# Performance work log

Hardware: AMD Instinct MI355X
Metric: run time of the kernel (lower is better)

The kernel has to match this reference:

```python
import jax, jax.numpy as jnp
import numpy as np

N_HEADS = 8
D_HEAD = 64  # n_embd=512 / n_heads=8


def setup_inputs() -> dict:
    key = jax.random.key(0)
    ks = jax.random.split(key, 5)
    B, T, C = 2, 4096, 512
    x = jax.random.normal(ks[0], (B, T, C), dtype=jnp.float32)
    s = 1.0 / np.sqrt(C)
    Wq = jax.random.normal(ks[1], (C, C), dtype=jnp.float32) * s
    Wk = jax.random.normal(ks[2], (C, C), dtype=jnp.float32) * s
    Wv = jax.random.normal(ks[3], (C, C), dtype=jnp.float32) * s
    Wout = jax.random.normal(ks[4], (C, C), dtype=jnp.float32) * s
    return {"x": x, "Wq": Wq, "Wk": Wk, "Wv": Wv, "Wout": Wout}


def reference(x, Wq, Wk, Wv, Wout):
    # x: [B,T,C]; nn.Linear(y) = y @ W.T, here weights stored as [C,C] used directly
    B, T, C = x.shape
    H, D = N_HEADS, D_HEAD
    q = (x @ Wq.T).reshape(B, T, H, D).transpose(0, 2, 1, 3)  # [B,H,T,D]
    k = (x @ Wk.T).reshape(B, T, H, D).transpose(0, 2, 1, 3)
    v = (x @ Wv.T).reshape(B, T, H, D).transpose(0, 2, 1, 3)
    att = jnp.einsum('bhqd,bhkd->bhqk', q, k) / jnp.sqrt(jnp.float32(D))  # [B,H,T,T]
    causal = jnp.tril(jnp.ones((T, T), dtype=bool))
    att = jnp.where(causal, att, -jnp.inf)
    att = jax.nn.softmax(att, axis=-1)
    # dropout is identity in eval mode (p=0)
    y = jnp.einsum('bhqk,bhkd->bhqd', att, v)  # [B,H,T,D]
    y = y.transpose(0, 2, 1, 3).reshape(B, T, C)
    return y @ Wout.T
```

## Files before the change

kernel.cpp:

```cpp
#include <hip/hip_runtime.h>
#include <hip/hip_bf16.h>
#include <math.h>
#include <stdint.h>

using bf16 = __hip_bfloat16;
typedef __attribute__((ext_vector_type(8))) short short8;
typedef __attribute__((ext_vector_type(4))) short short4v;
typedef __attribute__((ext_vector_type(4))) float float4v;

#define MFMA16(a, b, c) __builtin_amdgcn_mfma_f32_16x16x32_bf16(a, b, c, 0, 0, 0)

__device__ __forceinline__ short bfbits(float f) {
  bf16 h = (bf16)f;
  return *(short*)&h;
}

__device__ __forceinline__ short8 ld_cvt8(const float* p) {
  union { float4v v[2]; float f[8]; } u;
  u.v[0] = *(const float4v*)p;
  u.v[1] = *(const float4v*)(p + 4);
  short8 r;
#pragma unroll
  for (int j = 0; j < 8; j++) r[j] = bfbits(u.f[j]);
  return r;
}

__device__ __forceinline__ void gload16(const bf16* g, bf16* l) {
  __builtin_amdgcn_global_load_lds(
      (const __attribute__((address_space(1))) void*)g,
      (__attribute__((address_space(3))) void*)l, 16, 0, 0);
}

__global__ __launch_bounds__(256) void conv_all(
    const float* __restrict__ x, const float* __restrict__ w0,
    const float* __restrict__ w1, const float* __restrict__ w2,
    const float* __restrict__ w3, bf16* __restrict__ cx,
    bf16* __restrict__ cw) {
  size_t gid = ((size_t)blockIdx.x * 256 + threadIdx.x) * 8;
  const float* src;
  bf16* dst;
  size_t off;
  if (gid < 4194304) {
    src = x; dst = cx; off = gid;
  } else {
    size_t r = gid - 4194304;
    int wi = (int)(r >> 18);
    src = wi == 0 ? w0 : wi == 1 ? w1 : wi == 2 ? w2 : w3;
    dst = cw + ((size_t)wi << 18);
    off = r & 262143;
  }
  *(short8*)(dst + off) = ld_cvt8(src + off);
}

template <int MODE, int MT>
__device__ __forceinline__ void gemm_body(bf16* As, bf16* Bs,
                                          const bf16* __restrict__ A,
                                          const bf16* __restrict__ W,
                                          void* __restrict__ outp,
                                          float oscale) {
  constexpr int MI = MT / 32;
  const int bm = blockIdx.x * MT, bn = blockIdx.y * 128;
  const int tid = threadIdx.x;
  const int lane = tid & 63;
  const int wave = tid >> 6;
  const int lr = lane & 15, quad = lane >> 4;
  const int wm = (wave & 1) * (MT / 2), wn = (wave >> 1) * 64;

  const int srow = lane >> 3;
  const int scl = (lane & 7) ^ (srow & 7);
  const int rsw = lr & 7;

  float4v acc[MI][4] = {};

  for (int k0 = 0; k0 < 512; k0 += 64) {
    __syncthreads();
#pragma unroll
    for (int j = 0; j < MT / 32; j++) {
      const int m = wave + 4 * j;
      gload16(&A[(size_t)(bm + 8 * m + srow) * 512 + k0 + scl * 8],
              &As[(8 * m) * 64]);
    }
#pragma unroll
    for (int j = 0; j < 4; j++) {
      const int m = wave + 4 * j;
      gload16(&W[(size_t)(bn + 8 * m + srow) * 512 + k0 + scl * 8],
              &Bs[(8 * m) * 64]);
    }
    __syncthreads();
#pragma unroll
    for (int kk = 0; kk < 2; kk++) {
      short8 af[MI], bfv[4];
#pragma unroll
      for (int i = 0; i < MI; i++)
        af[i] = *(const short8*)
            &As[(wm + i * 16 + lr) * 64 + ((4 * kk + quad) ^ rsw) * 8];
#pragma unroll
      for (int i = 0; i < 4; i++)
        bfv[i] = *(const short8*)
            &Bs[(wn + i * 16 + lr) * 64 + ((4 * kk + quad) ^ rsw) * 8];
#pragma unroll
      for (int mi = 0; mi < MI; mi++)
#pragma unroll
        for (int ni = 0; ni < 4; ni++)
          acc[mi][ni] = MFMA16(af[mi], bfv[ni], acc[mi][ni]);
    }
  }

  const int row0 = bm + wm + quad * 4;
  const int col0 = bn + wn + lr;
#pragma unroll
  for (int mi = 0; mi < MI; mi++) {
#pragma unroll
    for (int ni = 0; ni < 4; ni++) {
      const int col = col0 + ni * 16;
      if (MODE == 1) {
        float* out = (float*)outp;
#pragma unroll
        for (int i = 0; i < 4; i++) {
          int m = row0 + mi * 16 + i;
          out[(size_t)m * 512 + col] = acc[mi][ni][i];
        }
      } else if (MODE == 0) {
        bf16* out = (bf16*)outp;
        const int hh = col >> 6, d = col & 63;
#pragma unroll
        for (int i = 0; i < 4; i++) {
          int m = row0 + mi * 16 + i;
          int bb = m >> 12, t = m & 4095;
          out[(((size_t)(bb * 8 + hh) * 4096 + t) << 6) + d] =
              (bf16)(acc[mi][ni][i] * oscale);
        }
      } else {
        bf16* out = (bf16*)outp;
        const int hh = col >> 6, d = col & 63;
        int m0 = row0 + mi * 16;
        int bb = m0 >> 12, t0 = m0 & 4095;
        short4v pk;
#pragma unroll
        for (int i = 0; i < 4; i++) pk[i] = bfbits(acc[mi][ni][i]);
        *(short4v*)&out[(((size_t)(bb * 8 + hh) * 64 + d) << 12) + t0] = pk;
      }
    }
  }
}

#define QSCALE 0.18033688f

__global__ __launch_bounds__(256) void qkv_kernel(
    const bf16* __restrict__ cx, const bf16* __restrict__ cW,
    bf16* q, bf16* k, bf16* vt) {
  __shared__ __align__(16) bf16 As[128 * 64];
  __shared__ __align__(16) bf16 Bs[128 * 64];
  if (blockIdx.z == 0)      gemm_body<0, 128>(As, Bs, cx, cW, q, QSCALE);
  else if (blockIdx.z == 1) gemm_body<0, 128>(As, Bs, cx, cW + 262144, k, 1.0f);
  else                      gemm_body<2, 128>(As, Bs, cx, cW + 2 * 262144, vt, 1.0f);
}

__global__ __launch_bounds__(256) void proj_kernel(
    const bf16* __restrict__ y, const bf16* __restrict__ cWout,
    float* __restrict__ out) {
  __shared__ __align__(16) bf16 As[64 * 64];
  __shared__ __align__(16) bf16 Bs[128 * 64];
  gemm_body<1, 64>(As, Bs, y, cWout, out, 1.0f);
}

__device__ __forceinline__ int lsw(int row, int col) {
  return (row << 6) + (col ^ ((row & 7) << 3));
}

template <bool DIAG>
__device__ __forceinline__ void attn_step(const bf16* __restrict__ Kc,
                                          const bf16* __restrict__ Vc,
                                          short8 qf0, short8 qf1, short8 ones,
                                          int wave, int lr, int quad,
                                          float4v& Lacc, float4v* O) {
  float4v S[4] = {};
#pragma unroll
  for (int nc = 0; nc < 4; nc++) {
    short8 kf0 = *(const short8*)&Kc[lsw(nc * 16 + lr, quad * 8)];
    short8 kf1 = *(const short8*)&Kc[lsw(nc * 16 + lr, 32 + quad * 8)];
    S[nc] = MFMA16(kf0, qf0, S[nc]);
    S[nc] = MFMA16(kf1, qf1, S[nc]);
  }

  short8 pf0, pf1;
#pragma unroll
  for (int nc = 0; nc < 4; nc++) {
#pragma unroll
    for (int i = 0; i < 4; i++) {
      float pv = exp2f(S[nc][i]);
      if (DIAG) {
        int kl = nc * 16 + quad * 4 + i;
        pv = (kl > wave * 16 + lr) ? 0.f : pv;
      }
      short bb = bfbits(pv);
      if (nc == 0)      pf0[i] = bb;
      else if (nc == 1) pf0[4 + i] = bb;
      else if (nc == 2) pf1[i] = bb;
      else              pf1[4 + i] = bb;
    }
  }

  Lacc = MFMA16(pf0, ones, Lacc);
  Lacc = MFMA16(pf1, ones, Lacc);

#pragma unroll
  for (int nc = 0; nc < 4; nc++) {
    const int row = nc * 16 + lr;
    short8 vfa = *(const short8*)&Vc[lsw(row, quad * 8)];
    short8 vfb = *(const short8*)&Vc[lsw(row, 32 + quad * 8)];
    O[nc] = MFMA16(pf0, vfa, O[nc]);
    O[nc] = MFMA16(pf1, vfb, O[nc]);
  }
}

__device__ __forceinline__ void vstore_perm(bf16* Vb, int row, int vA,
                                            short8 rv) {
  short4v lo = __builtin_shufflevector(rv, rv, 0, 1, 2, 3);
  short4v hi = __builtin_shufflevector(rv, rv, 4, 5, 6, 7);
  *(short4v*)&Vb[lsw(row, vA)] = lo;
  *(short4v*)&Vb[lsw(row, vA + 8)] = hi;
}

__global__ __launch_bounds__(512, 4) void attn_kernel(const bf16* __restrict__ Qg,
                                                      const bf16* __restrict__ Kg,
                                                      const bf16* __restrict__ Vtg,
                                                      bf16* __restrict__ Y) {
  constexpr int T = 4096;
  __shared__ __align__(16) bf16 KV[2][2][2][64 * 64];

  const int bx = blockIdx.x;
  const int qt = 63 - (bx >> 4);
  const int hb = bx & 15;
  const int h = hb >> 1, b = hb & 1;
  const size_t ho = ((size_t)(b * 8 + h)) * T * 64;
  const bf16* Qh = Qg + ho;
  const bf16* Kh = Kg + ho;
  const bf16* Vth = Vtg + ho;

  const int tid = threadIdx.x;
  const int G = tid >> 8;
  const int t = tid & 255;
  const int wave = t >> 6, lane = t & 63;
  const int lr = lane & 15, quad = lane >> 4;

  const int S0 = (qt + 2) >> 1;
  const int S1 = qt + 1 - S0;
  const int kbase = G ? S0 : 0;
  const int mysteps = G ? S1 : S0;

  bf16* const Kb0 = KV[G][0][0];
  bf16* const Kb1 = KV[G][1][0];
  bf16* const Vb0 = KV[G][0][1];
  bf16* const Vb1 = KV[G][1][1];

  const int sr = t >> 3;
  const int s8 = t & 7;
  const int sc = s8 * 8;
  const int vA = 32 * (s8 >> 2) + 16 * (s8 & 1) + 4 * ((s8 >> 1) & 1);
  const bf16* ksrc0 = Kh + (size_t)sr * 64 + sc;
  const bf16* ksrc1 = ksrc0 + 32 * 64;
  const bf16* vsrc0 = Vth + (size_t)sr * T + sc;
  const bf16* vsrc1 = vsrc0 + (size_t)32 * T;
  const int d0 = lsw(sr, sc);
  const int d1 = lsw(sr + 32, sc);

  short8 rk0, rk1, rv0, rv1;
  if (mysteps > 0) {
    const size_t ko = (size_t)kbase * 4096;
    const size_t vo = (size_t)kbase * 64;
    rk0 = *(const short8*)(ksrc0 + ko);
    rk1 = *(const short8*)(ksrc1 + ko);
    rv0 = *(const short8*)(vsrc0 + vo);
    rv1 = *(const short8*)(vsrc1 + vo);
  }

  {
    int rr = tid >> 3, c = (tid & 7) * 8;
    *(short8*)&KV[0][1][0][lsw(rr, c)] =
        *(const short8*)&Qh[(size_t)(qt * 64 + rr) * 64 + c];
  }
  __syncthreads();
  short8 qf0 = *(const short8*)&KV[0][1][0][lsw(wave * 16 + lr, quad * 8)];
  short8 qf1 = *(const short8*)&KV[0][1][0][lsw(wave * 16 + lr, 32 + quad * 8)];
  if (mysteps > 0) {
    *(short8*)&Kb0[d0] = rk0;
    *(short8*)&Kb0[d1] = rk1;
    vstore_perm(Vb0, sr, vA, rv0);
    vstore_perm(Vb0, sr + 32, vA, rv1);
  }
  __syncthreads();

  short8 ones;
#pragma unroll
  for (int j = 0; j < 8; j++) ones[j] = (short)0x3F80;

  float4v O[4] = {};
  float4v Lacc = {};

  for (int s = 0; s < S0; s++) {
    const bool act = s < mysteps;
    const bool pf = s + 1 < mysteps;
    if (pf) {
      const size_t ko = (size_t)(kbase + s + 1) * 4096;
      const size_t vo = (size_t)(kbase + s + 1) * 64;
      rk0 = *(const short8*)(ksrc0 + ko);
      rk1 = *(const short8*)(ksrc1 + ko);
      rv0 = *(const short8*)(vsrc0 + vo);
      rv1 = *(const short8*)(vsrc1 + vo);
    }

    if (act) {
      const bf16* Kc = (s & 1) ? Kb1 : Kb0;
      const bf16* Vc = (s & 1) ? Vb1 : Vb0;
      const int kt = kbase + s;
      if (kt == qt) attn_step<true>(Kc, Vc, qf0, qf1, ones, wave, lr, quad, Lacc, O);
      else          attn_step<false>(Kc, Vc, qf0, qf1, ones, wave, lr, quad, Lacc, O);
    }

    if (pf) {
      bf16* Kn = (s & 1) ? Kb0 : Kb1;
      bf16* Vn = (s & 1) ? Vb0 : Vb1;
      *(short8*)&Kn[d0] = rk0;
      *(short8*)&Kn[d1] = rk1;
      vstore_perm(Vn, sr, vA, rv0);
      vstore_perm(Vn, sr + 32, vA, rv1);
    }
    __syncthreads();
  }

  float* Op = (float*)&KV[1][0][0][0];
  float* Lp = Op + 64 * 64;
  const int r0 = wave * 16 + quad * 4;
  if (G == 1 && S1 > 0) {
#pragma unroll
    for (int nc = 0; nc < 4; nc++)
#pragma unroll
      for (int i = 0; i < 4; i++)
        Op[(r0 + i) * 64 + nc * 16 + lr] = O[nc][i];
    if (lr == 0) {
#pragma unroll
      for (int i = 0; i < 4; i++) Lp[r0 + i] = Lacc[i];
    }
  }
  __syncthreads();
  if (G == 0) {
    float inv[4];
#pragma unroll
    for (int i = 0; i < 4; i++) {
      float lt = Lacc[i] + (S1 > 0 ? Lp[r0 + i] : 0.f);
      inv[i] = 1.f / lt;
    }
    const size_t yb = ((size_t)b * T + qt * 64 + r0) * 512 + h * 64;
#pragma unroll
    for (int nc = 0; nc < 4; nc++)
#pragma unroll
      for (int i = 0; i < 4; i++) {
        float o = O[nc][i] + (S1 > 0 ? Op[(r0 + i) * 64 + nc * 16 + lr] : 0.f);
        Y[yb + (size_t)i * 512 + nc * 16 + lr] = (bf16)(o * inv[i]);
      }
  }
}

extern "C" void kernel_launch(void* const* d_in, const int* in_sizes, int n_in,
                              void* d_out, int out_size, void* d_ws, size_t ws_size,
                              hipStream_t stream) {
  (void)out_size; (void)ws_size;
  const int NX = 8192 * 512;
  int xi = 0;
  for (int i = 0; i < n_in; i++)
    if (in_sizes[i] == NX) { xi = i; break; }
  const float* x = (const float*)d_in[xi];
  const float* wsrc[4];
  int wn = 0;
  for (int i = 0; i < n_in && wn < 4; i++)
    if (i != xi) wsrc[wn++] = (const float*)d_in[i];

  bf16* ws = (bf16*)d_ws;
  const size_t HE = (size_t)NX;
  bf16* q  = ws;
  bf16* k  = q + HE;
  bf16* yx = k + HE;
  bf16* cw = yx + HE;
  bf16* vt = (bf16*)d_out;
  float* out = (float*)d_out;

  conv_all<<<2560, 256, 0, stream>>>(x, wsrc[0], wsrc[1], wsrc[2], wsrc[3],
                                     yx, cw);
  qkv_kernel<<<dim3(64, 4, 3), 256, 0, stream>>>(yx, cw, q, k, vt);
  attn_kernel<<<1024, 512, 0, stream>>>(q, k, vt, yx);
  proj_kernel<<<dim3(128, 4), 256, 0, stream>>>(yx, cw + 3 * 262144, out);
}
```

Before: 165.5 us.

## Give each attention wave two 16-row query tiles, halving block threads

The attention kernel drops from 512 to 256 threads per block, with 2 waves per key-split group instead of 4. Each wave now handles 32 query rows as two 16-row sub-tiles, so each K and V fragment read from shared memory feeds twice as many MFMAs. Each thread also loads twice as many K/V rows per step. The aim is less LDS read traffic per MFMA and more independent MFMA chains per wave. In exchange, accumulator registers and the per-thread load work double, and fewer waves per block are available to hide latency.

```diff
diff --git a/kernel.cpp b/kernel.cpp
--- a/kernel.cpp
+++ b/kernel.cpp
@@ -169,48 +169,57 @@
 }
 
 template <bool DIAG>
-__device__ __forceinline__ void attn_step(const bf16* __restrict__ Kc,
-                                          const bf16* __restrict__ Vc,
-                                          short8 qf0, short8 qf1, short8 ones,
-                                          int wave, int lr, int quad,
-                                          float4v& Lacc, float4v* O) {
-  float4v S[4] = {};
+__device__ __forceinline__ void attn_step2(const bf16* __restrict__ Kc,
+                                           const bf16* __restrict__ Vc,
+                                           const short8 (&qf)[2][2],
+                                           short8 ones, int qb ,
+                                           int lr, int quad,
+                                           float4v (&Lacc)[2],
+                                           float4v (&O)[2][4]) {
+  float4v S[2][4] = {};
 #pragma unroll
   for (int nc = 0; nc < 4; nc++) {
     short8 kf0 = *(const short8*)&Kc[lsw(nc * 16 + lr, quad * 8)];
     short8 kf1 = *(const short8*)&Kc[lsw(nc * 16 + lr, 32 + quad * 8)];
-    S[nc] = MFMA16(kf0, qf0, S[nc]);
-    S[nc] = MFMA16(kf1, qf1, S[nc]);
-  }
-
-  short8 pf0, pf1;
+#pragma unroll
+    for (int s = 0; s < 2; s++) {
+      S[s][nc] = MFMA16(kf0, qf[s][0], S[s][nc]);
+      S[s][nc] = MFMA16(kf1, qf[s][1], S[s][nc]);
+    }
+  }
+
+  short8 pf[2][2];
+#pragma unroll
+  for (int s = 0; s < 2; s++) {
+#pragma unroll
+    for (int nc = 0; nc < 4; nc++) {
+#pragma unroll
+      for (int i = 0; i < 4; i++) {
+        float pv = exp2f(S[s][nc][i]);
+        if (DIAG) {
+          int kl = nc * 16 + quad * 4 + i;
+          pv = (kl > qb + 16 * s + lr) ? 0.f : pv;
+        }
+        short bb = bfbits(pv);
+        if (nc == 0)      pf[s][0][i] = bb;
+        else if (nc == 1) pf[s][0][4 + i] = bb;
+        else if (nc == 2) pf[s][1][i] = bb;
+        else              pf[s][1][4 + i] = bb;
+      }
+    }
+    Lacc[s] = MFMA16(pf[s][0], ones, Lacc[s]);
+    Lacc[s] = MFMA16(pf[s][1], ones, Lacc[s]);
+  }
+
 #pragma unroll
   for (int nc = 0; nc < 4; nc++) {
-#pragma unroll
-    for (int i = 0; i < 4; i++) {
-      float pv = exp2f(S[nc][i]);
-      if (DIAG) {
-        int kl = nc * 16 + quad * 4 + i;
-        pv = (kl > wave * 16 + lr) ? 0.f : pv;
-      }
-      short bb = bfbits(pv);
-      if (nc == 0)      pf0[i] = bb;
-      else if (nc == 1) pf0[4 + i] = bb;
-      else if (nc == 2) pf1[i] = bb;
-      else              pf1[4 + i] = bb;
-    }
-  }
-
-  Lacc = MFMA16(pf0, ones, Lacc);
-  Lacc = MFMA16(pf1, ones, Lacc);
-
-#pragma unroll
-  for (int nc = 0; nc < 4; nc++) {
-    const int row = nc * 16 + lr;
-    short8 vfa = *(const short8*)&Vc[lsw(row, quad * 8)];
-    short8 vfb = *(const short8*)&Vc[lsw(row, 32 + quad * 8)];
-    O[nc] = MFMA16(pf0, vfa, O[nc]);
-    O[nc] = MFMA16(pf1, vfb, O[nc]);
+    short8 vfa = *(const short8*)&Vc[lsw(nc * 16 + lr, quad * 8)];
+    short8 vfb = *(const short8*)&Vc[lsw(nc * 16 + lr, 32 + quad * 8)];
+#pragma unroll
+    for (int s = 0; s < 2; s++) {
+      O[s][nc] = MFMA16(pf[s][0], vfa, O[s][nc]);
+      O[s][nc] = MFMA16(pf[s][1], vfb, O[s][nc]);
+    }
   }
 }
 
@@ -222,7 +231,7 @@
   *(short4v*)&Vb[lsw(row, vA + 8)] = hi;
 }
 
-__global__ __launch_bounds__(512, 4) void attn_kernel(const bf16* __restrict__ Qg,
+__global__ __launch_bounds__(256, 2) void attn_kernel(const bf16* __restrict__ Qg,
                                                       const bf16* __restrict__ Kg,
                                                       const bf16* __restrict__ Vtg,
                                                       bf16* __restrict__ Y) {
@@ -239,10 +248,11 @@
   const bf16* Vth = Vtg + ho;
 
   const int tid = threadIdx.x;
-  const int G = tid >> 8;
-  const int t = tid & 255;
+  const int G = tid >> 7;
+  const int t = tid & 127;
   const int wave = t >> 6, lane = t & 63;
   const int lr = lane & 15, quad = lane >> 4;
+  const int qb = wave * 32;
 
   const int S0 = (qt + 2) >> 1;
   const int S1 = qt + 1 - S0;
@@ -258,36 +268,46 @@
   const int s8 = t & 7;
   const int sc = s8 * 8;
   const int vA = 32 * (s8 >> 2) + 16 * (s8 & 1) + 4 * ((s8 >> 1) & 1);
-  const bf16* ksrc0 = Kh + (size_t)sr * 64 + sc;
-  const bf16* ksrc1 = ksrc0 + 32 * 64;
-  const bf16* vsrc0 = Vth + (size_t)sr * T + sc;
-  const bf16* vsrc1 = vsrc0 + (size_t)32 * T;
-  const int d0 = lsw(sr, sc);
-  const int d1 = lsw(sr + 32, sc);
-
-  short8 rk0, rk1, rv0, rv1;
+  const bf16* ksrc[4];
+  const bf16* vsrc[4];
+  int dK[4];
+#pragma unroll
+  for (int j = 0; j < 4; j++) {
+    ksrc[j] = Kh + (size_t)(sr + 16 * j) * 64 + sc;
+    vsrc[j] = Vth + (size_t)(sr + 16 * j) * T + sc;
+    dK[j] = lsw(sr + 16 * j, sc);
+  }
+
+  short8 rk[4], rv[4];
   if (mysteps > 0) {
     const size_t ko = (size_t)kbase * 4096;
     const size_t vo = (size_t)kbase * 64;
-    rk0 = *(const short8*)(ksrc0 + ko);
-    rk1 = *(const short8*)(ksrc1 + ko);
-    rv0 = *(const short8*)(vsrc0 + vo);
-    rv1 = *(const short8*)(vsrc1 + vo);
-  }
-
-  {
-    int rr = tid >> 3, c = (tid & 7) * 8;
+#pragma unroll
+    for (int j = 0; j < 4; j++) {
+      rk[j] = *(const short8*)(ksrc[j] + ko);
+      rv[j] = *(const short8*)(vsrc[j] + vo);
+    }
+  }
+
+#pragma unroll
+  for (int j = 0; j < 2; j++) {
+    int rr = (tid >> 3) + 32 * j, c = (tid & 7) * 8;
     *(short8*)&KV[0][1][0][lsw(rr, c)] =
         *(const short8*)&Qh[(size_t)(qt * 64 + rr) * 64 + c];
   }
   __syncthreads();
-  short8 qf0 = *(const short8*)&KV[0][1][0][lsw(wave * 16 + lr, quad * 8)];
-  short8 qf1 = *(const short8*)&KV[0][1][0][lsw(wave * 16 + lr, 32 + quad * 8)];
+  short8 qf[2][2];
+#pragma unroll
+  for (int s = 0; s < 2; s++) {
+    qf[s][0] = *(const short8*)&KV[0][1][0][lsw(qb + 16 * s + lr, quad * 8)];
+    qf[s][1] = *(const short8*)&KV[0][1][0][lsw(qb + 16 * s + lr, 32 + quad * 8)];
+  }
   if (mysteps > 0) {
-    *(short8*)&Kb0[d0] = rk0;
-    *(short8*)&Kb0[d1] = rk1;
-    vstore_perm(Vb0, sr, vA, rv0);
-    vstore_perm(Vb0, sr + 32, vA, rv1);
+#pragma unroll
+    for (int j = 0; j < 4; j++) {
+      *(short8*)&Kb0[dK[j]] = rk[j];
+      vstore_perm(Vb0, sr + 16 * j, vA, rv[j]);
+    }
   }
   __syncthreads();
 
@@ -295,8 +315,8 @@
 #pragma unroll
   for (int j = 0; j < 8; j++) ones[j] = (short)0x3F80;
 
-  float4v O[4] = {};
-  float4v Lacc = {};
+  float4v O[2][4] = {};
+  float4v Lacc[2] = {};
 
   for (int s = 0; s < S0; s++) {
     const bool act = s < mysteps;
@@ -304,61 +324,71 @@
     if (pf) {
       const size_t ko = (size_t)(kbase + s + 1) * 4096;
       const size_t vo = (size_t)(kbase + s + 1) * 64;
-      rk0 = *(const short8*)(ksrc0 + ko);
-      rk1 = *(const short8*)(ksrc1 + ko);
-      rv0 = *(const short8*)(vsrc0 + vo);
-      rv1 = *(const short8*)(vsrc1 + vo);
+#pragma unroll
+      for (int j = 0; j < 4; j++) {
+        rk[j] = *(const short8*)(ksrc[j] + ko);
+        rv[j] = *(const short8*)(vsrc[j] + vo);
+      }
     }
 
     if (act) {
       const bf16* Kc = (s & 1) ? Kb1 : Kb0;
       const bf16* Vc = (s & 1) ? Vb1 : Vb0;
       const int kt = kbase + s;
-      if (kt == qt) attn_step<true>(Kc, Vc, qf0, qf1, ones, wave, lr, quad, Lacc, O);
-      else          attn_step<false>(Kc, Vc, qf0, qf1, ones, wave, lr, quad, Lacc, O);
+      if (kt == qt) attn_step2<true>(Kc, Vc, qf, ones, qb, lr, quad, Lacc, O);
+      else          attn_step2<false>(Kc, Vc, qf, ones, qb, lr, quad, Lacc, O);
     }
 
     if (pf) {
       bf16* Kn = (s & 1) ? Kb0 : Kb1;
       bf16* Vn = (s & 1) ? Vb0 : Vb1;
-      *(short8*)&Kn[d0] = rk0;
-      *(short8*)&Kn[d1] = rk1;
-      vstore_perm(Vn, sr, vA, rv0);
-      vstore_perm(Vn, sr + 32, vA, rv1);
+#pragma unroll
+      for (int j = 0; j < 4; j++) {
+        *(short8*)&Kn[dK[j]] = rk[j];
+        vstore_perm(Vn, sr + 16 * j, vA, rv[j]);
+      }
     }
     __syncthreads();
   }
 
   float* Op = (float*)&KV[1][0][0][0];
-  float* Lp = Op + 64 * 64;
-  const int r0 = wave * 16 + quad * 4;
+  float* Lp = (float*)&KV[1][1][0][0];
   if (G == 1 && S1 > 0) {
 #pragma unroll
-    for (int nc = 0; nc < 4; nc++)
-#pragma unroll
-      for (int i = 0; i < 4; i++)
-        Op[(r0 + i) * 64 + nc * 16 + lr] = O[nc][i];
-    if (lr == 0) {
-#pragma unroll
-      for (int i = 0; i < 4; i++) Lp[r0 + i] = Lacc[i];
+    for (int s = 0; s < 2; s++) {
+      const int r0 = qb + 16 * s + quad * 4;
+#pragma unroll
+      for (int nc = 0; nc < 4; nc++)
+#pragma unroll
+        for (int i = 0; i < 4; i++)
+          Op[(r0 + i) * 64 + nc * 16 + lr] = O[s][nc][i];
+      if (lr == 0) {
+#pragma unroll
+        for (int i = 0; i < 4; i++) Lp[r0 + i] = Lacc[s][i];
+      }
     }
   }
   __syncthreads();
   if (G == 0) {
-    float inv[4];
-#pragma unroll
-    for (int i = 0; i < 4; i++) {
-      float lt = Lacc[i] + (S1 > 0 ? Lp[r0 + i] : 0.f);
-      inv[i] = 1.f / lt;
-    }
-    const size_t yb = ((size_t)b * T + qt * 64 + r0) * 512 + h * 64;
-#pragma unroll
-    for (int nc = 0; nc < 4; nc++)
+#pragma unroll
+    for (int s = 0; s < 2; s++) {
+      const int r0 = qb + 16 * s + quad * 4;
+      float inv[4];
 #pragma unroll
       for (int i = 0; i < 4; i++) {
-        float o = O[nc][i] + (S1 > 0 ? Op[(r0 + i) * 64 + nc * 16 + lr] : 0.f);
-        Y[yb + (size_t)i * 512 + nc * 16 + lr] = (bf16)(o * inv[i]);
-      }
+        float lt = Lacc[s][i] + (S1 > 0 ? Lp[r0 + i] : 0.f);
+        inv[i] = 1.f / lt;
+      }
+      const size_t yb = ((size_t)b * T + qt * 64 + r0) * 512 + h * 64;
+#pragma unroll
+      for (int nc = 0; nc < 4; nc++)
+#pragma unroll
+        for (int i = 0; i < 4; i++) {
+          float o = O[s][nc][i] +
+                    (S1 > 0 ? Op[(r0 + i) * 64 + nc * 16 + lr] : 0.f);
+          Y[yb + (size_t)i * 512 + nc * 16 + lr] = (bf16)(o * inv[i]);
+        }
+    }
   }
 }
 
@@ -388,6 +418,6 @@
   conv_all<<<2560, 256, 0, stream>>>(x, wsrc[0], wsrc[1], wsrc[2], wsrc[3],
                                      yx, cw);
   qkv_kernel<<<dim3(64, 4, 3), 256, 0, stream>>>(yx, cw, q, k, vt);
-  attn_kernel<<<1024, 512, 0, stream>>>(q, k, vt, yx);
+  attn_kernel<<<1024, 256, 0, stream>>>(q, k, vt, yx);
   proj_kernel<<<dim3(128, 4), 256, 0, stream>>>(yx, cw + 3 * 262144, out);
 }
```

Result: no change. 164.9 us (-0.4%).

## Pair complementary causal query tiles per block to balance attention work

Applied to the files above, without the earlier changes.

Each attention block now handles two query tiles, p and 63-p, so every block processes exactly 65 key tiles, split evenly between its two 256-thread groups. The grid shrinks from 1024 to 512 blocks. This removes the load imbalance of causal attention, where early query tiles finish quickly and late ones dominate the tail. In exchange each thread holds twice the accumulator and Q-fragment registers, and there are half as many blocks to hide latency with.

```diff
diff --git a/kernel.cpp b/kernel.cpp
--- a/kernel.cpp
+++ b/kernel.cpp
@@ -230,7 +230,8 @@
   __shared__ __align__(16) bf16 KV[2][2][2][64 * 64];
 
   const int bx = blockIdx.x;
-  const int qt = 63 - (bx >> 4);
+  const int p = bx >> 4;
+  const int pB = 63 - p;
   const int hb = bx & 15;
   const int h = hb >> 1, b = hb & 1;
   const size_t ho = ((size_t)(b * 8 + h)) * T * 64;
@@ -244,10 +245,13 @@
   const int wave = t >> 6, lane = t & 63;
   const int lr = lane & 15, quad = lane >> 4;
 
-  const int S0 = (qt + 2) >> 1;
-  const int S1 = qt + 1 - S0;
-  const int kbase = G ? S0 : 0;
-  const int mysteps = G ? S1 : S0;
+  const int hA = (p + 2) >> 1;
+  const int hB = (65 - p) >> 1;
+  const int myA = G ? (p + 1 - hA) : hA;
+  const int myB = G ? (64 - p - hB) : hB;
+  const int aB = G ? hA : 0;
+  const int bB = G ? hB : 0;
+  const int mysteps = myA + myB;
 
   bf16* const Kb0 = KV[G][0][0];
   bf16* const Kb1 = KV[G][1][0];
@@ -265,57 +269,62 @@
   const int d0 = lsw(sr, sc);
   const int d1 = lsw(sr + 32, sc);
 
-  short8 rk0, rk1, rv0, rv1;
-  if (mysteps > 0) {
-    const size_t ko = (size_t)kbase * 4096;
-    const size_t vo = (size_t)kbase * 64;
-    rk0 = *(const short8*)(ksrc0 + ko);
-    rk1 = *(const short8*)(ksrc1 + ko);
-    rv0 = *(const short8*)(vsrc0 + vo);
-    rv1 = *(const short8*)(vsrc1 + vo);
-  }
+  const int kt0 = (0 < myA) ? aB : bB;
+
+  short8 rk0 = *(const short8*)(ksrc0 + (size_t)kt0 * 4096);
+  short8 rk1 = *(const short8*)(ksrc1 + (size_t)kt0 * 4096);
+  short8 rv0 = *(const short8*)(vsrc0 + (size_t)kt0 * 64);
+  short8 rv1 = *(const short8*)(vsrc1 + (size_t)kt0 * 64);
 
   {
     int rr = tid >> 3, c = (tid & 7) * 8;
     *(short8*)&KV[0][1][0][lsw(rr, c)] =
-        *(const short8*)&Qh[(size_t)(qt * 64 + rr) * 64 + c];
+        *(const short8*)&Qh[(size_t)(p * 64 + rr) * 64 + c];
+    *(short8*)&KV[1][1][0][lsw(rr, c)] =
+        *(const short8*)&Qh[(size_t)(pB * 64 + rr) * 64 + c];
   }
   __syncthreads();
-  short8 qf0 = *(const short8*)&KV[0][1][0][lsw(wave * 16 + lr, quad * 8)];
-  short8 qf1 = *(const short8*)&KV[0][1][0][lsw(wave * 16 + lr, 32 + quad * 8)];
-  if (mysteps > 0) {
-    *(short8*)&Kb0[d0] = rk0;
-    *(short8*)&Kb0[d1] = rk1;
-    vstore_perm(Vb0, sr, vA, rv0);
-    vstore_perm(Vb0, sr + 32, vA, rv1);
-  }
+  short8 qfA0 = *(const short8*)&KV[0][1][0][lsw(wave * 16 + lr, quad * 8)];
+  short8 qfA1 = *(const short8*)&KV[0][1][0][lsw(wave * 16 + lr, 32 + quad * 8)];
+  short8 qfB0 = *(const short8*)&KV[1][1][0][lsw(wave * 16 + lr, quad * 8)];
+  short8 qfB1 = *(const short8*)&KV[1][1][0][lsw(wave * 16 + lr, 32 + quad * 8)];
+  *(short8*)&Kb0[d0] = rk0;
+  *(short8*)&Kb0[d1] = rk1;
+  vstore_perm(Vb0, sr, vA, rv0);
+  vstore_perm(Vb0, sr + 32, vA, rv1);
   __syncthreads();
 
   short8 ones;
 #pragma unroll
   for (int j = 0; j < 8; j++) ones[j] = (short)0x3F80;
 
-  float4v O[4] = {};
-  float4v Lacc = {};
-
-  for (int s = 0; s < S0; s++) {
+  float4v OA[4] = {}, OB[4] = {};
+  float4v LA = {}, LB = {};
+
+  for (int s = 0; s < 33; s++) {
     const bool act = s < mysteps;
     const bool pf = s + 1 < mysteps;
     if (pf) {
-      const size_t ko = (size_t)(kbase + s + 1) * 4096;
-      const size_t vo = (size_t)(kbase + s + 1) * 64;
-      rk0 = *(const short8*)(ksrc0 + ko);
-      rk1 = *(const short8*)(ksrc1 + ko);
-      rv0 = *(const short8*)(vsrc0 + vo);
-      rv1 = *(const short8*)(vsrc1 + vo);
+      const int sn = s + 1;
+      const int ktn = (sn < myA) ? (aB + sn) : (bB + (sn - myA));
+      rk0 = *(const short8*)(ksrc0 + (size_t)ktn * 4096);
+      rk1 = *(const short8*)(ksrc1 + (size_t)ktn * 4096);
+      rv0 = *(const short8*)(vsrc0 + (size_t)ktn * 64);
+      rv1 = *(const short8*)(vsrc1 + (size_t)ktn * 64);
     }
 
     if (act) {
       const bf16* Kc = (s & 1) ? Kb1 : Kb0;
       const bf16* Vc = (s & 1) ? Vb1 : Vb0;
-      const int kt = kbase + s;
-      if (kt == qt) attn_step<true>(Kc, Vc, qf0, qf1, ones, wave, lr, quad, Lacc, O);
-      else          attn_step<false>(Kc, Vc, qf0, qf1, ones, wave, lr, quad, Lacc, O);
+      if (s < myA) {
+        const int kt = aB + s;
+        if (kt == p) attn_step<true>(Kc, Vc, qfA0, qfA1, ones, wave, lr, quad, LA, OA);
+        else         attn_step<false>(Kc, Vc, qfA0, qfA1, ones, wave, lr, quad, LA, OA);
+      } else {
+        const int kt = bB + (s - myA);
+        if (kt == pB) attn_step<true>(Kc, Vc, qfB0, qfB1, ones, wave, lr, quad, LB, OB);
+        else          attn_step<false>(Kc, Vc, qfB0, qfB1, ones, wave, lr, quad, LB, OB);
+      }
     }
 
     if (pf) {
@@ -329,35 +338,42 @@
     __syncthreads();
   }
 
-  float* Op = (float*)&KV[1][0][0][0];
-  float* Lp = Op + 64 * 64;
+  float* OpA = (float*)&KV[1][0][0][0];
+  float* OpB = (float*)&KV[1][1][0][0];
+  float* LpA = (float*)&KV[0][0][0][0];
+  float* LpB = LpA + 64;
   const int r0 = wave * 16 + quad * 4;
-  if (G == 1 && S1 > 0) {
+  if (G == 1) {
 #pragma unroll
     for (int nc = 0; nc < 4; nc++)
 #pragma unroll
-      for (int i = 0; i < 4; i++)
-        Op[(r0 + i) * 64 + nc * 16 + lr] = O[nc][i];
+      for (int i = 0; i < 4; i++) {
+        OpA[(r0 + i) * 64 + nc * 16 + lr] = OA[nc][i];
+        OpB[(r0 + i) * 64 + nc * 16 + lr] = OB[nc][i];
+      }
     if (lr == 0) {
 #pragma unroll
-      for (int i = 0; i < 4; i++) Lp[r0 + i] = Lacc[i];
+      for (int i = 0; i < 4; i++) { LpA[r0 + i] = LA[i]; LpB[r0 + i] = LB[i]; }
     }
   }
   __syncthreads();
   if (G == 0) {
-    float inv[4];
+    float invA[4], invB[4];
 #pragma unroll
     for (int i = 0; i < 4; i++) {
-      float lt = Lacc[i] + (S1 > 0 ? Lp[r0 + i] : 0.f);
-      inv[i] = 1.f / lt;
-    }
-    const size_t yb = ((size_t)b * T + qt * 64 + r0) * 512 + h * 64;
+      invA[i] = 1.f / (LA[i] + LpA[r0 + i]);
+      invB[i] = 1.f / (LB[i] + LpB[r0 + i]);
+    }
+    const size_t ybA = ((size_t)b * T + p * 64 + r0) * 512 + h * 64;
+    const size_t ybB = ((size_t)b * T + pB * 64 + r0) * 512 + h * 64;
 #pragma unroll
     for (int nc = 0; nc < 4; nc++)
 #pragma unroll
       for (int i = 0; i < 4; i++) {
-        float o = O[nc][i] + (S1 > 0 ? Op[(r0 + i) * 64 + nc * 16 + lr] : 0.f);
-        Y[yb + (size_t)i * 512 + nc * 16 + lr] = (bf16)(o * inv[i]);
+        float oa = OA[nc][i] + OpA[(r0 + i) * 64 + nc * 16 + lr];
+        float ob = OB[nc][i] + OpB[(r0 + i) * 64 + nc * 16 + lr];
+        Y[ybA + (size_t)i * 512 + nc * 16 + lr] = (bf16)(oa * invA[i]);
+        Y[ybB + (size_t)i * 512 + nc * 16 + lr] = (bf16)(ob * invB[i]);
       }
   }
 }
@@ -388,6 +404,6 @@
   conv_all<<<2560, 256, 0, stream>>>(x, wsrc[0], wsrc[1], wsrc[2], wsrc[3],
                                      yx, cw);
   qkv_kernel<<<dim3(64, 4, 3), 256, 0, stream>>>(yx, cw, q, k, vt);
-  attn_kernel<<<1024, 512, 0, stream>>>(q, k, vt, yx);
+  attn_kernel<<<512, 512, 0, stream>>>(q, k, vt, yx);
   proj_kernel<<<dim3(128, 4), 256, 0, stream>>>(yx, cw + 3 * 262144, out);
 }
```

After: 161.5 us. -2.4%, faster.
